# Optimization experiments

Hardware: AMD Instinct MI355X
Metric: run time of the kernel (lower is better)

Reference implementation:

```python
import jax, jax.numpy as jnp
import numpy as np

H = 128  # hidden_dim
F = 64   # node_feat_dim


def setup_inputs() -> dict:
    key = jax.random.key(0)
    ks = jax.random.split(key, 24)
    N, E, NR, NT = 50000, 400000, 20000, 20000
    inp = {
        "mol_x": jax.random.normal(ks[0], (N, F), jnp.float32),
        "pos": jax.random.normal(ks[1], (N, 3), jnp.float32),
        "reaction_x": jax.random.normal(ks[2], (NR, F), jnp.float32),
        "target_x": jax.random.normal(ks[3], (NT, F), jnp.float32),
        "edge_index": jax.random.randint(ks[4], (2, E), 0, N, jnp.int32),
    }
    def lin(k, fan_in, fan_out):
        s = 1.0 / np.sqrt(fan_in)
        kw, kb = jax.random.split(k)
        W = jax.random.uniform(kw, (fan_in, fan_out), jnp.float32, -s, s)
        b = jax.random.uniform(kb, (fan_out,), jnp.float32, -s, s)
        return W, b
    inp["W_node"], inp["b_node"] = lin(ks[5], F, H)
    inp["W_att1"], inp["b_att1"] = lin(ks[6], 2 * H + 3, H)
    inp["W_att2"], inp["b_att2"] = lin(ks[7], H, 1)
    inp["W_upd"], inp["b_upd"] = lin(ks[8], H, H)
    inp["Wy1"], inp["by1"] = lin(ks[9], H, 64)
    inp["Wy2"], inp["by2"] = lin(ks[10], 64, 1)
    inp["Wa1"], inp["ba1"] = lin(ks[11], H, 64)
    inp["Wa2"], inp["ba2"] = lin(ks[12], 64, 1)
    return inp


def reference(mol_x, pos, reaction_x, target_x, edge_index,
              W_node, b_node, W_att1, b_att1, W_att2, b_att2,
              W_upd, b_upd, Wy1, by1, Wy2, by2, Wa1, ba1, Wa2, ba2):
    N = mol_x.shape[0]
    # node encoder
    h = mol_x @ W_node + b_node                      # [N, H]
    src, dst = edge_index[0], edge_index[1]          # PyG: x_j = source, x_i = target
    x_j = h[src]                                      # [E, H]
    x_i = h[dst]                                      # [E, H]
    dist = pos[dst] - pos[src]                        # [E, 3]
    cat = jnp.concatenate([x_i, x_j, dist], axis=1)   # [E, 2H+3]
    s = jax.nn.relu(cat @ W_att1 + b_att1) @ W_att2 + b_att2  # [E, 1]
    att = jax.nn.softmax(s, axis=0)                   # global softmax over edges (dim=0)
    msg = x_j * att                                   # [E, H]
    aggr = jax.ops.segment_sum(msg, dst, num_segments=N)  # scatter-add -> [N, H]
    mol_feats = aggr @ W_upd + b_upd                  # [N, H]
    # heads on reaction / target graphs
    rh = reaction_x @ W_node + b_node
    th = target_x @ W_node + b_node
    pred_yield = (jax.nn.relu(rh @ Wy1 + by1) @ Wy2 + by2).squeeze(-1)
    pred_activity = (jax.nn.relu(th @ Wa1 + ba1) @ Wa2 + ba2).squeeze(-1)
    return pred_yield, pred_activity, mol_feats
```

## Files before the change

### kernel.cpp

```cpp
#include <hip/hip_runtime.h>
#include <hip/hip_bf16.h>

typedef unsigned short ushort_t;
typedef __attribute__((ext_vector_type(8))) short s16x8;
typedef __attribute__((ext_vector_type(4))) float f32x4;

__device__ inline unsigned short f2bf(float x) {
    unsigned u = __float_as_uint(x);
    return (unsigned short)((u + 0x7FFFu + ((u >> 16) & 1u)) >> 16);
}
__device__ inline float bflo(unsigned u) { return __uint_as_float(u << 16); }
__device__ inline float bfhi(unsigned u) { return __uint_as_float(u & 0xffff0000u); }

__device__ inline void pack_one(const float* __restrict__ W, int K, int N,
                                ushort_t* __restrict__ dst, int g) {
    int KT = K / 32;
    int nt = g / (KT * 64);
    int rem = g % (KT * 64);
    int kt = rem / 64, lane = rem % 64;
    int n = nt * 16 + (lane & 15);
    int kbase = kt * 32 + ((lane >> 4) << 3);
    ushort_t tmp[8];
#pragma unroll
    for (int j = 0; j < 8; ++j) tmp[j] = f2bf(W[(size_t)(kbase + j) * N + n]);
    uint4 pk;
    pk.x = tmp[0] | ((unsigned)tmp[1] << 16);
    pk.y = tmp[2] | ((unsigned)tmp[3] << 16);
    pk.z = tmp[4] | ((unsigned)tmp[5] << 16);
    pk.w = tmp[6] | ((unsigned)tmp[7] << 16);
    *(uint4*)&dst[(size_t)g * 8] = pk;
}

__global__ void convert_w(const float* __restrict__ Wn, const float* __restrict__ W1,
                          const float* __restrict__ Wu, const float* __restrict__ Wy1,
                          const float* __restrict__ Wa1,
                          ushort_t* __restrict__ Wnb, ushort_t* __restrict__ W1tb,
                          ushort_t* __restrict__ W1mb, ushort_t* __restrict__ Wub,
                          ushort_t* __restrict__ Wy1b, ushort_t* __restrict__ Wa1b,
                          int* __restrict__ counts, int N) {
    int t = blockIdx.x * 256 + threadIdx.x;
    if (t < 1024)       pack_one(Wn, 64, 128, Wnb, t);
    else if (t < 3072)  pack_one(W1, 128, 128, W1tb, t - 1024);
    else if (t < 5120)  pack_one(W1 + 128 * 128, 128, 128, W1mb, t - 3072);
    else if (t < 7168)  pack_one(Wu, 128, 128, Wub, t - 5120);
    else if (t < 8192)  pack_one(Wy1, 128, 64, Wy1b, t - 7168);
    else if (t < 9216)  pack_one(Wa1, 128, 64, Wa1b, t - 8192);
    if (t < N) counts[t] = 0;
}

__global__ void encode_pq(const float* __restrict__ x, const ushort_t* __restrict__ Wnb,
                          const float* __restrict__ bn, const ushort_t* __restrict__ W1tb,
                          const ushort_t* __restrict__ W1mb, const float* __restrict__ b1,
                          ushort_t* __restrict__ hb, ushort_t* __restrict__ P,
                          ushort_t* __restrict__ Q, int nrows) {
    __shared__ ushort_t ldsH[4 * 16 * 136];
    int t = threadIdx.x;
    int w = t >> 6, lane = t & 63;
    int c = lane & 15, q = lane >> 4;
    int r0 = blockIdx.x * 64 + w * 16;
    int rowA = r0 + c; if (rowA >= nrows) rowA = nrows - 1;
    ushort_t* myH = &ldsH[w * 16 * 136];

    s16x8 xa[2];
#pragma unroll
    for (int kt = 0; kt < 2; ++kt) {
        const float* xp = &x[(size_t)rowA * 64 + kt * 32 + q * 8];
        float4 v0 = *(const float4*)xp;
        float4 v1 = *(const float4*)(xp + 4);
        s16x8 a;
        a[0] = (short)f2bf(v0.x); a[1] = (short)f2bf(v0.y);
        a[2] = (short)f2bf(v0.z); a[3] = (short)f2bf(v0.w);
        a[4] = (short)f2bf(v1.x); a[5] = (short)f2bf(v1.y);
        a[6] = (short)f2bf(v1.z); a[7] = (short)f2bf(v1.w);
        xa[kt] = a;
    }
#pragma unroll
    for (int nt = 0; nt < 8; ++nt) {
        f32x4 acc = {0.f, 0.f, 0.f, 0.f};
#pragma unroll
        for (int kt = 0; kt < 2; ++kt) {
            s16x8 b = *(const s16x8*)&Wnb[((nt * 2 + kt) * 64 + lane) * 8];
            acc = __builtin_amdgcn_mfma_f32_16x16x32_bf16(xa[kt], b, acc, 0, 0, 0);
        }
        float bi = bn[nt * 16 + c];
#pragma unroll
        for (int r = 0; r < 4; ++r) {
            int row = r0 + q * 4 + r;
            ushort_t hv = f2bf(acc[r] + bi);
            myH[(q * 4 + r) * 136 + nt * 16 + c] = hv;
            if (row < nrows) hb[(size_t)row * 128 + nt * 16 + c] = hv;
        }
    }
    __syncthreads();
    s16x8 ha[4];
#pragma unroll
    for (int kt = 0; kt < 4; ++kt)
        ha[kt] = *(const s16x8*)&myH[c * 136 + kt * 32 + q * 8];
#pragma unroll
    for (int nt = 0; nt < 8; ++nt) {
        f32x4 pa = {0.f, 0.f, 0.f, 0.f}, qa = pa;
#pragma unroll
        for (int kt = 0; kt < 4; ++kt) {
            s16x8 bp = *(const s16x8*)&W1tb[((nt * 4 + kt) * 64 + lane) * 8];
            s16x8 bq = *(const s16x8*)&W1mb[((nt * 4 + kt) * 64 + lane) * 8];
            pa = __builtin_amdgcn_mfma_f32_16x16x32_bf16(ha[kt], bp, pa, 0, 0, 0);
            qa = __builtin_amdgcn_mfma_f32_16x16x32_bf16(ha[kt], bq, qa, 0, 0, 0);
        }
        float bi = b1[nt * 16 + c];
#pragma unroll
        for (int r = 0; r < 4; ++r) {
            int row = r0 + q * 4 + r;
            if (row < nrows) {
                P[(size_t)row * 128 + nt * 16 + c] = f2bf(pa[r] + bi);
                Q[(size_t)row * 128 + nt * 16 + c] = f2bf(qa[r]);
            }
        }
    }
}

__global__ void edge_score(const ushort_t* __restrict__ P, const ushort_t* __restrict__ Q,
                           const float* __restrict__ pos, const int* __restrict__ src,
                           const int* __restrict__ dst, const float* __restrict__ W1b,
                           const float* __restrict__ W2, const float* __restrict__ b2,
                           float* __restrict__ s_out, int* __restrict__ counts,
                           float* __restrict__ redm, float* __restrict__ rede, int E) {
    __shared__ float wsh[4 * 128];
    __shared__ float smm[256], sme[256];
    int t = threadIdx.x;
    for (int i = t; i < 384; i += 256) wsh[i] = W1b[i];
    if (t < 128) wsh[384 + t] = W2[t];
    __syncthreads();
    int w = t >> 6, lane = t & 63;
    int g = lane >> 4, c = lane & 15;
    float w0[8], w1[8], w2[8], wv[8];
#pragma unroll
    for (int j = 0; j < 8; ++j) {
        w0[j] = wsh[c * 8 + j];
        w1[j] = wsh[128 + c * 8 + j];
        w2[j] = wsh[256 + c * 8 + j];
        wv[j] = wsh[384 + c * 8 + j];
    }
    float b2v = b2[0];
    int base = blockIdx.x * 64 + w * 16;
    float m = -1e30f, ev = 0.f;

    int sa[4], da[4];
#pragma unroll
    for (int it = 0; it < 4; ++it) {
        int e = base + it * 4 + g;
        int ee = (e < E) ? e : (E - 1);
        sa[it] = src[ee]; da[it] = dst[ee];
    }
    uint4 pr[4], qr[4];
    float dd0[4], dd1[4], dd2[4];
#pragma unroll
    for (int it = 0; it < 4; ++it) {
        pr[it] = *(const uint4*)&P[(size_t)da[it] * 128 + c * 8];
        qr[it] = *(const uint4*)&Q[(size_t)sa[it] * 128 + c * 8];
        dd0[it] = pos[da[it] * 3]     - pos[sa[it] * 3];
        dd1[it] = pos[da[it] * 3 + 1] - pos[sa[it] * 3 + 1];
        dd2[it] = pos[da[it] * 3 + 2] - pos[sa[it] * 3 + 2];
    }
#pragma unroll
    for (int it = 0; it < 4; ++it) {
        int e = base + it * 4 + g;
        bool valid = e < E;
        unsigned pw[4] = {pr[it].x, pr[it].y, pr[it].z, pr[it].w};
        unsigned qw[4] = {qr[it].x, qr[it].y, qr[it].z, qr[it].w};
        float d0 = dd0[it], d1 = dd1[it], d2 = dd2[it];
        float v = 0.f;
#pragma unroll
        for (int jj = 0; jj < 4; ++jj) {
            float pe = bflo(pw[jj]) + bflo(qw[jj])
                     + d0 * w0[2 * jj] + d1 * w1[2 * jj] + d2 * w2[2 * jj];
            float po = bfhi(pw[jj]) + bfhi(qw[jj])
                     + d0 * w0[2 * jj + 1] + d1 * w1[2 * jj + 1] + d2 * w2[2 * jj + 1];
            v += fmaxf(pe, 0.f) * wv[2 * jj] + fmaxf(po, 0.f) * wv[2 * jj + 1];
        }
#pragma unroll
        for (int off = 1; off < 16; off <<= 1) v += __shfl_xor(v, off, 64);
        float sv = v + b2v;
        if (c == 0 && valid) {
            s_out[e] = sv;
            atomicAdd(&counts[da[it]], 1);
            float nm = fmaxf(m, sv);
            ev = ev * __expf(m - nm) + __expf(sv - nm);
            m = nm;
        }
    }
    smm[t] = m; sme[t] = ev; __syncthreads();
    for (int off = 128; off > 0; off >>= 1) {
        if (t < off) {
            float m1 = smm[t], m2 = smm[t + off];
            float e1 = sme[t], e2 = sme[t + off];
            float M = fmaxf(m1, m2);
            smm[t] = M;
            sme[t] = e1 * __expf(m1 - M) + e2 * __expf(m2 - M);
        }
        __syncthreads();
    }
    if (t == 0) { redm[blockIdx.x] = smm[0]; rede[blockIdx.x] = sme[0]; }
}

__global__ void smax2(const float* __restrict__ redm, const float* __restrict__ rede,
                      float* __restrict__ scal, int nb) {
    __shared__ float smm[256], sme[256];
    int t = threadIdx.x;
    float m = -1e30f, ev = 0.f;
    for (int i = t; i < nb; i += 256) {
        float m2 = redm[i], e2 = rede[i];
        float M = fmaxf(m, m2);
        ev = ev * __expf(m - M) + e2 * __expf(m2 - M);
        m = M;
    }
    smm[t] = m; sme[t] = ev; __syncthreads();
    for (int off = 128; off > 0; off >>= 1) {
        if (t < off) {
            float m1 = smm[t], m2 = smm[t + off];
            float e1 = sme[t], e2 = sme[t + off];
            float M = fmaxf(m1, m2);
            smm[t] = M;
            sme[t] = e1 * __expf(m1 - M) + e2 * __expf(m2 - M);
        }
        __syncthreads();
    }
    if (t == 0) { scal[0] = smm[0]; scal[1] = 1.f / sme[0]; }
}

__global__ void scan1(const int* __restrict__ counts, int* __restrict__ offs,
                      int* __restrict__ partials, int N) {
    __shared__ int sm[256];
    int i = blockIdx.x * 256 + threadIdx.x;
    int v = (i < N) ? counts[i] : 0;
    sm[threadIdx.x] = v; __syncthreads();
    for (int off = 1; off < 256; off <<= 1) {
        int add = (threadIdx.x >= off) ? sm[threadIdx.x - off] : 0;
        __syncthreads();
        sm[threadIdx.x] += add;
        __syncthreads();
    }
    if (i < N) offs[i] = sm[threadIdx.x] - v;
    if (threadIdx.x == 255) partials[blockIdx.x] = sm[255];
}

__global__ void scan_add(int* __restrict__ offs, int* __restrict__ cursor,
                         const int* __restrict__ partials, int nb, int N) {
    __shared__ int sm[256];
    int t = threadIdx.x;
    sm[t] = (t < nb && t < blockIdx.x) ? partials[t] : 0;
    __syncthreads();
    for (int off = 128; off > 0; off >>= 1) {
        if (t < off) sm[t] += sm[t + off];
        __syncthreads();
    }
    int basev = sm[0];
    int i = blockIdx.x * 256 + t;
    if (i < N) {
        int v = offs[i] + basev;
        offs[i] = v;
        cursor[i] = v;
    }
}

__global__ void fill_csr(const int* __restrict__ src, const int* __restrict__ dst,
                         const float* __restrict__ s, int* __restrict__ cursor,
                         int2* __restrict__ csr, int E) {
    int e = blockIdx.x * 256 + threadIdx.x;
    if (e >= E) return;
    int p = atomicAdd(&cursor[dst[e]], 1);
    csr[p] = make_int2(src[e], __float_as_int(s[e]));
}

__global__ void gather_upd(const ushort_t* __restrict__ hb, const int2* __restrict__ csr,
                           const int* __restrict__ offs, const int* __restrict__ deg,
                           const float* __restrict__ scal,
                           const ushort_t* __restrict__ Wub, const float* __restrict__ bu,
                           float* __restrict__ C, int N) {
    __shared__ ushort_t ldsA[16 * 136];
    int t = threadIdx.x;
    int w = t >> 6, lane = t & 63;
    int g = lane >> 4, c = lane & 15;
    int r0 = blockIdx.x * 16;
    float m = scal[0], inv = scal[1];
#pragma unroll
    for (int i = 0; i < 4; ++i) {
        int node = r0 + w * 4 + i;
        float a[8] = {0.f, 0.f, 0.f, 0.f, 0.f, 0.f, 0.f, 0.f};
        if (node < N) {
            int start = offs[node], d = deg[node];
            for (int k = g; k < d; k += 4) {
                int2 v = csr[start + k];
                float att = __expf(__int_as_float(v.y) - m) * inv;
                uint4 hq = *(const uint4*)&hb[(size_t)v.x * 128 + c * 8];
                a[0] += bflo(hq.x) * att; a[1] += bfhi(hq.x) * att;
                a[2] += bflo(hq.y) * att; a[3] += bfhi(hq.y) * att;
                a[4] += bflo(hq.z) * att; a[5] += bfhi(hq.z) * att;
                a[6] += bflo(hq.w) * att; a[7] += bfhi(hq.w) * att;
            }
        }
#pragma unroll
        for (int j = 0; j < 8; ++j) {
            a[j] += __shfl_xor(a[j], 16, 64);
            a[j] += __shfl_xor(a[j], 32, 64);
        }
        if (g == 0) {
            uint4 pk;
            pk.x = f2bf(a[0]) | ((unsigned)f2bf(a[1]) << 16);
            pk.y = f2bf(a[2]) | ((unsigned)f2bf(a[3]) << 16);
            pk.z = f2bf(a[4]) | ((unsigned)f2bf(a[5]) << 16);
            pk.w = f2bf(a[6]) | ((unsigned)f2bf(a[7]) << 16);
            *(uint4*)&ldsA[(w * 4 + i) * 136 + c * 8] = pk;
        }
    }
    __syncthreads();
    int q = lane >> 4;
    int ntA = w, ntB = w + 4;
    f32x4 acc0 = {0.f, 0.f, 0.f, 0.f}, acc1 = acc0;
#pragma unroll
    for (int kt = 0; kt < 4; ++kt) {
        s16x8 av = *(const s16x8*)&ldsA[c * 136 + kt * 32 + q * 8];
        s16x8 b0 = *(const s16x8*)&Wub[((ntA * 4 + kt) * 64 + lane) * 8];
        s16x8 b1 = *(const s16x8*)&Wub[((ntB * 4 + kt) * 64 + lane) * 8];
        acc0 = __builtin_amdgcn_mfma_f32_16x16x32_bf16(av, b0, acc0, 0, 0, 0);
        acc1 = __builtin_amdgcn_mfma_f32_16x16x32_bf16(av, b1, acc1, 0, 0, 0);
    }
    float bi0 = bu[ntA * 16 + c], bi1 = bu[ntB * 16 + c];
#pragma unroll
    for (int r = 0; r < 4; ++r) {
        int row = r0 + q * 4 + r;
        if (row < N) {
            C[(size_t)row * 128 + ntA * 16 + c] = acc0[r] + bi0;
            C[(size_t)row * 128 + ntB * 16 + c] = acc1[r] + bi1;
        }
    }
}

__global__ void head_mfma(const float* __restrict__ rx, const float* __restrict__ tx,
                          const ushort_t* __restrict__ Wnb, const float* __restrict__ bn,
                          const ushort_t* __restrict__ Wy1b, const float* __restrict__ by1,
                          const float* __restrict__ Wy2, const float* __restrict__ by2,
                          const ushort_t* __restrict__ Wa1b, const float* __restrict__ ba1,
                          const float* __restrict__ Wa2, const float* __restrict__ ba2,
                          float* __restrict__ out, int nb1, int NR, int NT) {
    __shared__ ushort_t ldsA[16 * 72];
    __shared__ ushort_t ldsB[16 * 136];
    __shared__ float part[64];
    int blk = blockIdx.x;
    const float* x; const ushort_t* W1b; const float* b1; const float* W2; const float* b2;
    float* o; int r0, nrows;
    if (blk < nb1) { x = rx; W1b = Wy1b; b1 = by1; W2 = Wy2; b2 = by2; o = out; r0 = blk * 16; nrows = NR; }
    else { x = tx; W1b = Wa1b; b1 = ba1; W2 = Wa2; b2 = ba2; o = out + NR; r0 = (blk - nb1) * 16; nrows = NT; }

    int t = threadIdx.x;
    {
        int row = t >> 4, c4 = (t & 15) * 4;
        float4 v = *(const float4*)&x[(size_t)(r0 + row) * 64 + c4];
        uint2 pk;
        pk.x = f2bf(v.x) | ((unsigned)f2bf(v.y) << 16);
        pk.y = f2bf(v.z) | ((unsigned)f2bf(v.w) << 16);
        *(uint2*)&ldsA[row * 72 + c4] = pk;
    }
    __syncthreads();
    int w = t >> 6, lane = t & 63;
    int c = lane & 15, q = lane >> 4;
    {
        int ntA = w, ntB = w + 4;
        f32x4 acc0 = {0.f, 0.f, 0.f, 0.f}, acc1 = acc0;
#pragma unroll
        for (int kt = 0; kt < 2; ++kt) {
            s16x8 a = *(const s16x8*)&ldsA[c * 72 + kt * 32 + q * 8];
            s16x8 b0 = *(const s16x8*)&Wnb[((ntA * 2 + kt) * 64 + lane) * 8];
            s16x8 b1v = *(const s16x8*)&Wnb[((ntB * 2 + kt) * 64 + lane) * 8];
            acc0 = __builtin_amdgcn_mfma_f32_16x16x32_bf16(a, b0, acc0, 0, 0, 0);
            acc1 = __builtin_amdgcn_mfma_f32_16x16x32_bf16(a, b1v, acc1, 0, 0, 0);
        }
        float bi0 = bn[ntA * 16 + c], bi1 = bn[ntB * 16 + c];
#pragma unroll
        for (int r = 0; r < 4; ++r) {
            int row = q * 4 + r;
            ldsB[row * 136 + ntA * 16 + c] = f2bf(acc0[r] + bi0);
            ldsB[row * 136 + ntB * 16 + c] = f2bf(acc1[r] + bi1);
        }
    }
    __syncthreads();
    {
        f32x4 acc = {0.f, 0.f, 0.f, 0.f};
#pragma unroll
        for (int kt = 0; kt < 4; ++kt) {
            s16x8 a = *(const s16x8*)&ldsB[c * 136 + kt * 32 + q * 8];
            s16x8 b0 = *(const s16x8*)&W1b[((w * 4 + kt) * 64 + lane) * 8];
            acc = __builtin_amdgcn_mfma_f32_16x16x32_bf16(a, b0, acc, 0, 0, 0);
        }
        float bi = b1[w * 16 + c], w2v = W2[w * 16 + c];
#pragma unroll
        for (int r = 0; r < 4; ++r) {
            float u = fmaxf(acc[r] + bi, 0.f) * w2v;
#pragma unroll
            for (int mm = 1; mm < 16; mm <<= 1) u += __shfl_xor(u, mm, 64);
            if (c == 0) part[w * 16 + q * 4 + r] = u;
        }
    }
    __syncthreads();
    if (t < 16) {
        int row = r0 + t;
        if (row < nrows)
            o[row] = part[t] + part[16 + t] + part[32 + t] + part[48 + t] + b2[0];
    }
}

extern "C" void kernel_launch(void* const* d_in, const int* in_sizes, int n_in,
                              void* d_out, int out_size, void* d_ws, size_t ws_size,
                              hipStream_t stream) {
    const float* mol_x      = (const float*)d_in[0];
    const float* pos        = (const float*)d_in[1];
    const float* reaction_x = (const float*)d_in[2];
    const float* target_x   = (const float*)d_in[3];
    const int*   ei         = (const int*)d_in[4];
    const float* W_node = (const float*)d_in[5];
    const float* b_node = (const float*)d_in[6];
    const float* W_att1 = (const float*)d_in[7];
    const float* b_att1 = (const float*)d_in[8];
    const float* W_att2 = (const float*)d_in[9];
    const float* b_att2 = (const float*)d_in[10];
    const float* W_upd  = (const float*)d_in[11];
    const float* b_upd  = (const float*)d_in[12];
    const float* Wy1 = (const float*)d_in[13];
    const float* by1 = (const float*)d_in[14];
    const float* Wy2 = (const float*)d_in[15];
    const float* by2 = (const float*)d_in[16];
    const float* Wa1 = (const float*)d_in[17];
    const float* ba1 = (const float*)d_in[18];
    const float* Wa2 = (const float*)d_in[19];
    const float* ba2 = (const float*)d_in[20];

    int N  = in_sizes[0] / 64;
    int E  = in_sizes[4] / 2;
    int NR = in_sizes[2] / 64;
    int NT = in_sizes[3] / 64;

    float* out = (float*)d_out;

    int nbE = (E + 63) / 64;

    char* wp = (char*)d_ws;
    ushort_t* hb = (ushort_t*)wp;  wp += (size_t)N * 128 * 2;
    ushort_t* Qb = (ushort_t*)wp;  wp += (size_t)N * 128 * 2;
    float* s     = (float*)wp;     wp += (size_t)E * 4;
    float* redm  = (float*)wp;     wp += (size_t)nbE * 4;
    float* rede  = (float*)wp;     wp += (size_t)nbE * 4;
    float* scal  = (float*)wp;     wp += 4 * 4;
    int* counts  = (int*)wp;       wp += (size_t)N * 4;
    int* offs    = (int*)wp;       wp += (size_t)N * 4;
    int* cursor  = (int*)wp;       wp += (size_t)N * 4;
    int* partials= (int*)wp;       wp += 256 * 4;
    int2* csr    = (int2*)wp;      wp += (size_t)E * 8;
    ushort_t* Wnb  = (ushort_t*)wp; wp += 8192 * 2;
    ushort_t* W1tb = (ushort_t*)wp; wp += 16384 * 2;
    ushort_t* W1mb = (ushort_t*)wp; wp += 16384 * 2;
    ushort_t* Wub  = (ushort_t*)wp; wp += 16384 * 2;
    ushort_t* Wy1b = (ushort_t*)wp; wp += 8192 * 2;
    ushort_t* Wa1b = (ushort_t*)wp; wp += 8192 * 2;
    ushort_t* Pb = (ushort_t*)(out + NR + NT);
    float* molf  = out + NR + NT;

    const int* srcp = ei;
    const int* dstp = ei + E;
    int nbN = (N + 255) / 256;

    convert_w<<<nbN, 256, 0, stream>>>(W_node, W_att1, W_upd, Wy1, Wa1,
                                       Wnb, W1tb, W1mb, Wub, Wy1b, Wa1b, counts, N);
    encode_pq<<<(N + 63) / 64, 256, 0, stream>>>(mol_x, Wnb, b_node, W1tb, W1mb, b_att1,
                                                 hb, Pb, Qb, N);
    edge_score<<<nbE, 256, 0, stream>>>(Pb, Qb, pos, srcp, dstp,
                                        W_att1 + 256 * 128, W_att2, b_att2,
                                        s, counts, redm, rede, E);
    smax2<<<1, 256, 0, stream>>>(redm, rede, scal, nbE);
    scan1<<<nbN, 256, 0, stream>>>(counts, offs, partials, N);
    scan_add<<<nbN, 256, 0, stream>>>(offs, cursor, partials, nbN, N);
    fill_csr<<<(E + 255) / 256, 256, 0, stream>>>(srcp, dstp, s, cursor, csr, E);
    gather_upd<<<(N + 15) / 16, 256, 0, stream>>>(hb, csr, offs, counts, scal,
                                                  Wub, b_upd, molf, N);
    head_mfma<<<(NR + NT) / 16, 256, 0, stream>>>(reaction_x, target_x, Wnb, b_node,
                                                  Wy1b, by1, Wy2, by2, Wa1b, ba1, Wa2, ba2,
                                                  out, NR / 16, NR, NT);
}
```

Measured before the change: 249.3 us.

## Fuse edge scoring into CSR gather with per-node online softmax

Removes the separate edge_score pass: attention scores are now computed inside the destination-sorted gather, which keeps a per-node running max and sum and rescales the aggregated features. A global softmax rescale factor per node is applied after the W_upd MFMA, and the degree counting moves into encode_pq. Q and h are interleaved in one row so each source gather touches a single 512-byte region, and the CSR stores only source indices. The trade-off is a serialized per-node loop doing more exp work, a larger per-source read, and the risk of underflow in the per-node scaling for nodes whose max is far below the global max.

```diff
diff --git a/kernel.cpp b/kernel.cpp
--- a/kernel.cpp
+++ b/kernel.cpp
@@ -51,10 +51,13 @@
 __global__ void encode_pq(const float* __restrict__ x, const ushort_t* __restrict__ Wnb,
                           const float* __restrict__ bn, const ushort_t* __restrict__ W1tb,
                           const ushort_t* __restrict__ W1mb, const float* __restrict__ b1,
-                          ushort_t* __restrict__ hb, ushort_t* __restrict__ P,
-                          ushort_t* __restrict__ Q, int nrows) {
+                          ushort_t* __restrict__ QH, ushort_t* __restrict__ P,
+                          const int* __restrict__ dst, int* __restrict__ counts,
+                          int nrows, int E) {
     __shared__ ushort_t ldsH[4 * 16 * 136];
     int t = threadIdx.x;
+    for (int e = blockIdx.x * 256 + t; e < E; e += gridDim.x * 256)
+        atomicAdd(&counts[dst[e]], 1);
     int w = t >> 6, lane = t & 63;
     int c = lane & 15, q = lane >> 4;
     int r0 = blockIdx.x * 64 + w * 16;
@@ -88,7 +91,7 @@
             int row = r0 + q * 4 + r;
             ushort_t hv = f2bf(acc[r] + bi);
             myH[(q * 4 + r) * 136 + nt * 16 + c] = hv;
-            if (row < nrows) hb[(size_t)row * 128 + nt * 16 + c] = hv;
+            if (row < nrows) QH[(size_t)row * 256 + 128 + nt * 16 + c] = hv;
         }
     }
     __syncthreads();
@@ -112,119 +115,10 @@
             int row = r0 + q * 4 + r;
             if (row < nrows) {
                 P[(size_t)row * 128 + nt * 16 + c] = f2bf(pa[r] + bi);
-                Q[(size_t)row * 128 + nt * 16 + c] = f2bf(qa[r]);
+                QH[(size_t)row * 256 + nt * 16 + c] = f2bf(qa[r]);
             }
         }
     }
-}
-
-__global__ void edge_score(const ushort_t* __restrict__ P, const ushort_t* __restrict__ Q,
-                           const float* __restrict__ pos, const int* __restrict__ src,
-                           const int* __restrict__ dst, const float* __restrict__ W1b,
-                           const float* __restrict__ W2, const float* __restrict__ b2,
-                           float* __restrict__ s_out, int* __restrict__ counts,
-                           float* __restrict__ redm, float* __restrict__ rede, int E) {
-    __shared__ float wsh[4 * 128];
-    __shared__ float smm[256], sme[256];
-    int t = threadIdx.x;
-    for (int i = t; i < 384; i += 256) wsh[i] = W1b[i];
-    if (t < 128) wsh[384 + t] = W2[t];
-    __syncthreads();
-    int w = t >> 6, lane = t & 63;
-    int g = lane >> 4, c = lane & 15;
-    float w0[8], w1[8], w2[8], wv[8];
-#pragma unroll
-    for (int j = 0; j < 8; ++j) {
-        w0[j] = wsh[c * 8 + j];
-        w1[j] = wsh[128 + c * 8 + j];
-        w2[j] = wsh[256 + c * 8 + j];
-        wv[j] = wsh[384 + c * 8 + j];
-    }
-    float b2v = b2[0];
-    int base = blockIdx.x * 64 + w * 16;
-    float m = -1e30f, ev = 0.f;
-
-    int sa[4], da[4];
-#pragma unroll
-    for (int it = 0; it < 4; ++it) {
-        int e = base + it * 4 + g;
-        int ee = (e < E) ? e : (E - 1);
-        sa[it] = src[ee]; da[it] = dst[ee];
-    }
-    uint4 pr[4], qr[4];
-    float dd0[4], dd1[4], dd2[4];
-#pragma unroll
-    for (int it = 0; it < 4; ++it) {
-        pr[it] = *(const uint4*)&P[(size_t)da[it] * 128 + c * 8];
-        qr[it] = *(const uint4*)&Q[(size_t)sa[it] * 128 + c * 8];
-        dd0[it] = pos[da[it] * 3]     - pos[sa[it] * 3];
-        dd1[it] = pos[da[it] * 3 + 1] - pos[sa[it] * 3 + 1];
-        dd2[it] = pos[da[it] * 3 + 2] - pos[sa[it] * 3 + 2];
-    }
-#pragma unroll
-    for (int it = 0; it < 4; ++it) {
-        int e = base + it * 4 + g;
-        bool valid = e < E;
-        unsigned pw[4] = {pr[it].x, pr[it].y, pr[it].z, pr[it].w};
-        unsigned qw[4] = {qr[it].x, qr[it].y, qr[it].z, qr[it].w};
-        float d0 = dd0[it], d1 = dd1[it], d2 = dd2[it];
-        float v = 0.f;
-#pragma unroll
-        for (int jj = 0; jj < 4; ++jj) {
-            float pe = bflo(pw[jj]) + bflo(qw[jj])
-                     + d0 * w0[2 * jj] + d1 * w1[2 * jj] + d2 * w2[2 * jj];
-            float po = bfhi(pw[jj]) + bfhi(qw[jj])
-                     + d0 * w0[2 * jj + 1] + d1 * w1[2 * jj + 1] + d2 * w2[2 * jj + 1];
-            v += fmaxf(pe, 0.f) * wv[2 * jj] + fmaxf(po, 0.f) * wv[2 * jj + 1];
-        }
-#pragma unroll
-        for (int off = 1; off < 16; off <<= 1) v += __shfl_xor(v, off, 64);
-        float sv = v + b2v;
-        if (c == 0 && valid) {
-            s_out[e] = sv;
-            atomicAdd(&counts[da[it]], 1);
-            float nm = fmaxf(m, sv);
-            ev = ev * __expf(m - nm) + __expf(sv - nm);
-            m = nm;
-        }
-    }
-    smm[t] = m; sme[t] = ev; __syncthreads();
-    for (int off = 128; off > 0; off >>= 1) {
-        if (t < off) {
-            float m1 = smm[t], m2 = smm[t + off];
-            float e1 = sme[t], e2 = sme[t + off];
-            float M = fmaxf(m1, m2);
-            smm[t] = M;
-            sme[t] = e1 * __expf(m1 - M) + e2 * __expf(m2 - M);
-        }
-        __syncthreads();
-    }
-    if (t == 0) { redm[blockIdx.x] = smm[0]; rede[blockIdx.x] = sme[0]; }
-}
-
-__global__ void smax2(const float* __restrict__ redm, const float* __restrict__ rede,
-                      float* __restrict__ scal, int nb) {
-    __shared__ float smm[256], sme[256];
-    int t = threadIdx.x;
-    float m = -1e30f, ev = 0.f;
-    for (int i = t; i < nb; i += 256) {
-        float m2 = redm[i], e2 = rede[i];
-        float M = fmaxf(m, m2);
-        ev = ev * __expf(m - M) + e2 * __expf(m2 - M);
-        m = M;
-    }
-    smm[t] = m; sme[t] = ev; __syncthreads();
-    for (int off = 128; off > 0; off >>= 1) {
-        if (t < off) {
-            float m1 = smm[t], m2 = smm[t + off];
-            float e1 = sme[t], e2 = sme[t + off];
-            float M = fmaxf(m1, m2);
-            smm[t] = M;
-            sme[t] = e1 * __expf(m1 - M) + e2 * __expf(m2 - M);
-        }
-        __syncthreads();
-    }
-    if (t == 0) { scal[0] = smm[0]; scal[1] = 1.f / sme[0]; }
 }
 
 __global__ void scan1(const int* __restrict__ counts, int* __restrict__ offs,
@@ -263,57 +157,166 @@
 }
 
 __global__ void fill_csr(const int* __restrict__ src, const int* __restrict__ dst,
-                         const float* __restrict__ s, int* __restrict__ cursor,
-                         int2* __restrict__ csr, int E) {
+                         int* __restrict__ cursor, int* __restrict__ csrc, int E) {
     int e = blockIdx.x * 256 + threadIdx.x;
     if (e >= E) return;
     int p = atomicAdd(&cursor[dst[e]], 1);
-    csr[p] = make_int2(src[e], __float_as_int(s[e]));
-}
-
-__global__ void gather_upd(const ushort_t* __restrict__ hb, const int2* __restrict__ csr,
-                           const int* __restrict__ offs, const int* __restrict__ deg,
-                           const float* __restrict__ scal,
-                           const ushort_t* __restrict__ Wub, const float* __restrict__ bu,
-                           float* __restrict__ C, int N) {
-    __shared__ ushort_t ldsA[16 * 136];
-    int t = threadIdx.x;
+    csrc[p] = src[e];
+}
+
+__global__ void fused_gather(const ushort_t* __restrict__ P, const ushort_t* __restrict__ QH,
+                             const float* __restrict__ pos, const int* __restrict__ csrc,
+                             const int* __restrict__ offs, const int* __restrict__ deg,
+                             const float* __restrict__ W1b, const float* __restrict__ W2,
+                             const float* __restrict__ b2,
+                             ushort_t* __restrict__ A_out, float* __restrict__ m_out,
+                             float* __restrict__ redm, float* __restrict__ rede, int N) {
+    __shared__ float wsh[512];
+    __shared__ float smm[256], sme[256];
+    int t = threadIdx.x;
+    for (int i = t; i < 384; i += 256) wsh[i] = W1b[i];
+    if (t < 128) wsh[384 + t] = W2[t];
+    __syncthreads();
     int w = t >> 6, lane = t & 63;
     int g = lane >> 4, c = lane & 15;
-    int r0 = blockIdx.x * 16;
-    float m = scal[0], inv = scal[1];
+    float w0[8], w1[8], w2[8], wv[8];
+#pragma unroll
+    for (int j = 0; j < 8; ++j) {
+        w0[j] = wsh[c * 8 + j];
+        w1[j] = wsh[128 + c * 8 + j];
+        w2[j] = wsh[256 + c * 8 + j];
+        wv[j] = wsh[384 + c * 8 + j];
+    }
+    float b2v = b2[0];
+    float mB = -1e30f, zB = 0.f;
 #pragma unroll
     for (int i = 0; i < 4; ++i) {
-        int node = r0 + w * 4 + i;
+        int node = blockIdx.x * 16 + w * 4 + i;
+        float m = -1e30f, z = 0.f;
         float a[8] = {0.f, 0.f, 0.f, 0.f, 0.f, 0.f, 0.f, 0.f};
         if (node < N) {
+            uint4 pr = *(const uint4*)&P[(size_t)node * 128 + c * 8];
+            float pv[8];
+            pv[0] = bflo(pr.x); pv[1] = bfhi(pr.x); pv[2] = bflo(pr.y); pv[3] = bfhi(pr.y);
+            pv[4] = bflo(pr.z); pv[5] = bfhi(pr.z); pv[6] = bflo(pr.w); pv[7] = bfhi(pr.w);
+            float pd0 = pos[node * 3], pd1 = pos[node * 3 + 1], pd2 = pos[node * 3 + 2];
             int start = offs[node], d = deg[node];
             for (int k = g; k < d; k += 4) {
-                int2 v = csr[start + k];
-                float att = __expf(__int_as_float(v.y) - m) * inv;
-                uint4 hq = *(const uint4*)&hb[(size_t)v.x * 128 + c * 8];
-                a[0] += bflo(hq.x) * att; a[1] += bfhi(hq.x) * att;
-                a[2] += bflo(hq.y) * att; a[3] += bfhi(hq.y) * att;
-                a[4] += bflo(hq.z) * att; a[5] += bfhi(hq.z) * att;
-                a[6] += bflo(hq.w) * att; a[7] += bfhi(hq.w) * att;
+                int sa = csrc[start + k];
+                const ushort_t* qhp = &QH[(size_t)sa * 256 + c * 8];
+                uint4 qr = *(const uint4*)qhp;
+                uint4 hr = *(const uint4*)(qhp + 128);
+                float d0 = pd0 - pos[sa * 3];
+                float d1 = pd1 - pos[sa * 3 + 1];
+                float d2 = pd2 - pos[sa * 3 + 2];
+                unsigned qw[4] = {qr.x, qr.y, qr.z, qr.w};
+                float v = 0.f;
+#pragma unroll
+                for (int jj = 0; jj < 4; ++jj) {
+                    float pe = pv[2 * jj] + bflo(qw[jj])
+                             + d0 * w0[2 * jj] + d1 * w1[2 * jj] + d2 * w2[2 * jj];
+                    float po = pv[2 * jj + 1] + bfhi(qw[jj])
+                             + d0 * w0[2 * jj + 1] + d1 * w1[2 * jj + 1] + d2 * w2[2 * jj + 1];
+                    v += fmaxf(pe, 0.f) * wv[2 * jj] + fmaxf(po, 0.f) * wv[2 * jj + 1];
+                }
+#pragma unroll
+                for (int off = 1; off < 16; off <<= 1) v += __shfl_xor(v, off, 64);
+                float s = v + b2v;
+                float nm = fmaxf(m, s);
+                float f  = __expf(m - nm);
+                float es = __expf(s - nm);
+                z = z * f + es;
+                m = nm;
+                float hv[8];
+                hv[0] = bflo(hr.x); hv[1] = bfhi(hr.x); hv[2] = bflo(hr.y); hv[3] = bfhi(hr.y);
+                hv[4] = bflo(hr.z); hv[5] = bfhi(hr.z); hv[6] = bflo(hr.w); hv[7] = bfhi(hr.w);
+#pragma unroll
+                for (int j = 0; j < 8; ++j) a[j] = a[j] * f + hv[j] * es;
             }
         }
 #pragma unroll
-        for (int j = 0; j < 8; ++j) {
-            a[j] += __shfl_xor(a[j], 16, 64);
-            a[j] += __shfl_xor(a[j], 32, 64);
-        }
-        if (g == 0) {
+        for (int off = 16; off <= 32; off <<= 1) {
+            float m2 = __shfl_xor(m, off, 64);
+            float z2 = __shfl_xor(z, off, 64);
+            float M = fmaxf(m, m2);
+            float e1 = __expf(m - M), e2 = __expf(m2 - M);
+#pragma unroll
+            for (int j = 0; j < 8; ++j) {
+                float a2 = __shfl_xor(a[j], off, 64);
+                a[j] = a[j] * e1 + a2 * e2;
+            }
+            z = z * e1 + z2 * e2;
+            m = M;
+        }
+        if (g == 0 && node < N) {
             uint4 pk;
             pk.x = f2bf(a[0]) | ((unsigned)f2bf(a[1]) << 16);
             pk.y = f2bf(a[2]) | ((unsigned)f2bf(a[3]) << 16);
             pk.z = f2bf(a[4]) | ((unsigned)f2bf(a[5]) << 16);
             pk.w = f2bf(a[6]) | ((unsigned)f2bf(a[7]) << 16);
-            *(uint4*)&ldsA[(w * 4 + i) * 136 + c * 8] = pk;
-        }
-    }
-    __syncthreads();
-    int q = lane >> 4;
+            *(uint4*)&A_out[(size_t)node * 128 + c * 8] = pk;
+            if (c == 0) {
+                m_out[node] = m;
+                float M = fmaxf(mB, m);
+                float e1 = __expf(mB - M), e2 = __expf(m - M);
+                zB = zB * e1 + z * e2;
+                mB = M;
+            }
+        }
+    }
+    smm[t] = mB; sme[t] = zB; __syncthreads();
+    for (int off = 128; off > 0; off >>= 1) {
+        if (t < off) {
+            float m1 = smm[t], m2 = smm[t + off];
+            float e1 = sme[t], e2 = sme[t + off];
+            float M = fmaxf(m1, m2);
+            smm[t] = M;
+            sme[t] = e1 * __expf(m1 - M) + e2 * __expf(m2 - M);
+        }
+        __syncthreads();
+    }
+    if (t == 0) { redm[blockIdx.x] = smm[0]; rede[blockIdx.x] = sme[0]; }
+}
+
+__global__ void combine(const float* __restrict__ redm, const float* __restrict__ rede,
+                        float* __restrict__ scal, int nb) {
+    __shared__ float smm[256], sme[256];
+    int t = threadIdx.x;
+    float m = -1e30f, ev = 0.f;
+    for (int i = t; i < nb; i += 256) {
+        float m2 = redm[i], e2 = rede[i];
+        float M = fmaxf(m, m2);
+        ev = ev * __expf(m - M) + e2 * __expf(m2 - M);
+        m = M;
+    }
+    smm[t] = m; sme[t] = ev; __syncthreads();
+    for (int off = 128; off > 0; off >>= 1) {
+        if (t < off) {
+            float m1 = smm[t], m2 = smm[t + off];
+            float e1 = sme[t], e2 = sme[t + off];
+            float M = fmaxf(m1, m2);
+            smm[t] = M;
+            sme[t] = e1 * __expf(m1 - M) + e2 * __expf(m2 - M);
+        }
+        __syncthreads();
+    }
+    if (t == 0) { scal[0] = smm[0]; scal[1] = 1.f / sme[0]; }
+}
+
+__global__ void upd_mfma(const ushort_t* __restrict__ A, const float* __restrict__ m_n,
+                         const float* __restrict__ scal,
+                         const ushort_t* __restrict__ Wub, const float* __restrict__ bu,
+                         float* __restrict__ C, int N) {
+    __shared__ ushort_t ldsA[16 * 136];
+    int t = threadIdx.x;
+    int r0 = blockIdx.x * 16;
+    {
+        int row = t >> 4, c8 = (t & 15) * 8;
+        *(uint4*)&ldsA[row * 136 + c8] = *(const uint4*)&A[(size_t)(r0 + row) * 128 + c8];
+    }
+    __syncthreads();
+    int w = t >> 6, lane = t & 63;
+    int c = lane & 15, q = lane >> 4;
     int ntA = w, ntB = w + 4;
     f32x4 acc0 = {0.f, 0.f, 0.f, 0.f}, acc1 = acc0;
 #pragma unroll
@@ -324,13 +327,15 @@
         acc0 = __builtin_amdgcn_mfma_f32_16x16x32_bf16(av, b0, acc0, 0, 0, 0);
         acc1 = __builtin_amdgcn_mfma_f32_16x16x32_bf16(av, b1, acc1, 0, 0, 0);
     }
+    float M = scal[0], invZ = scal[1];
     float bi0 = bu[ntA * 16 + c], bi1 = bu[ntB * 16 + c];
 #pragma unroll
     for (int r = 0; r < 4; ++r) {
         int row = r0 + q * 4 + r;
         if (row < N) {
-            C[(size_t)row * 128 + ntA * 16 + c] = acc0[r] + bi0;
-            C[(size_t)row * 128 + ntB * 16 + c] = acc1[r] + bi1;
+            float sc = __expf(m_n[row] - M) * invZ;
+            C[(size_t)row * 128 + ntA * 16 + c] = acc0[r] * sc + bi0;
+            C[(size_t)row * 128 + ntB * 16 + c] = acc1[r] * sc + bi1;
         }
     }
 }
@@ -440,20 +445,20 @@
 
     float* out = (float*)d_out;
 
-    int nbE = (E + 63) / 64;
+    int nbG = (N + 15) / 16;
 
     char* wp = (char*)d_ws;
-    ushort_t* hb = (ushort_t*)wp;  wp += (size_t)N * 128 * 2;
-    ushort_t* Qb = (ushort_t*)wp;  wp += (size_t)N * 128 * 2;
-    float* s     = (float*)wp;     wp += (size_t)E * 4;
-    float* redm  = (float*)wp;     wp += (size_t)nbE * 4;
-    float* rede  = (float*)wp;     wp += (size_t)nbE * 4;
+    ushort_t* QH = (ushort_t*)wp;  wp += (size_t)N * 256 * 2;
+    ushort_t* Ab = (ushort_t*)wp;  wp += (size_t)N * 128 * 2;
+    float* m_n   = (float*)wp;     wp += (size_t)N * 4;
+    float* redm  = (float*)wp;     wp += (size_t)nbG * 4;
+    float* rede  = (float*)wp;     wp += (size_t)nbG * 4;
     float* scal  = (float*)wp;     wp += 4 * 4;
     int* counts  = (int*)wp;       wp += (size_t)N * 4;
     int* offs    = (int*)wp;       wp += (size_t)N * 4;
     int* cursor  = (int*)wp;       wp += (size_t)N * 4;
     int* partials= (int*)wp;       wp += 256 * 4;
-    int2* csr    = (int2*)wp;      wp += (size_t)E * 8;
+    int* csrc    = (int*)wp;       wp += (size_t)E * 4;
     ushort_t* Wnb  = (ushort_t*)wp; wp += 8192 * 2;
     ushort_t* W1tb = (ushort_t*)wp; wp += 16384 * 2;
     ushort_t* W1mb = (ushort_t*)wp; wp += 16384 * 2;
@@ -470,16 +475,15 @@
     convert_w<<<nbN, 256, 0, stream>>>(W_node, W_att1, W_upd, Wy1, Wa1,
                                        Wnb, W1tb, W1mb, Wub, Wy1b, Wa1b, counts, N);
     encode_pq<<<(N + 63) / 64, 256, 0, stream>>>(mol_x, Wnb, b_node, W1tb, W1mb, b_att1,
-                                                 hb, Pb, Qb, N);
-    edge_score<<<nbE, 256, 0, stream>>>(Pb, Qb, pos, srcp, dstp,
-                                        W_att1 + 256 * 128, W_att2, b_att2,
-                                        s, counts, redm, rede, E);
-    smax2<<<1, 256, 0, stream>>>(redm, rede, scal, nbE);
+                                                 QH, Pb, dstp, counts, N, E);
     scan1<<<nbN, 256, 0, stream>>>(counts, offs, partials, N);
     scan_add<<<nbN, 256, 0, stream>>>(offs, cursor, partials, nbN, N);
-    fill_csr<<<(E + 255) / 256, 256, 0, stream>>>(srcp, dstp, s, cursor, csr, E);
-    gather_upd<<<(N + 15) / 16, 256, 0, stream>>>(hb, csr, offs, counts, scal,
-                                                  Wub, b_upd, molf, N);
+    fill_csr<<<(E + 255) / 256, 256, 0, stream>>>(srcp, dstp, cursor, csrc, E);
+    fused_gather<<<nbG, 256, 0, stream>>>(Pb, QH, pos, csrc, offs, counts,
+                                          W_att1 + 256 * 128, W_att2, b_att2,
+                                          Ab, m_n, redm, rede, N);
+    combine<<<1, 256, 0, stream>>>(redm, rede, scal, nbG);
+    upd_mfma<<<(N + 15) / 16, 256, 0, stream>>>(Ab, m_n, scal, Wub, b_upd, molf, N);
     head_mfma<<<(NR + NT) / 16, 256, 0, stream>>>(reaction_x, target_x, Wnb, b_node,
                                                   Wy1b, by1, Wy2, by2, Wa1b, ba1, Wa2, ba2,
                                                   out, NR / 16, NR, NT);
```

After: 268.0 us. 1.08x slower.

## Move degree counting into encoder and fuse CSR fill into edge scoring

Applied to the files above, without the earlier changes.

The per-destination degree histogram is now built with atomics inside the encoder kernel, and the scan runs before edge scoring. The edge-score kernel then writes (src, score) pairs straight into CSR slots, which removes the separate fill_csr kernel and the intermediate score buffer. The cost is extra atomic traffic in the encoder and scattered CSR writes inside the scoring kernel. The gather loop in edge_score was also restructured from batched loads into a per-iteration loop, which may reduce memory-level parallelism.

```diff
diff --git a/kernel.cpp b/kernel.cpp
--- a/kernel.cpp
+++ b/kernel.cpp
@@ -52,9 +52,12 @@
                           const float* __restrict__ bn, const ushort_t* __restrict__ W1tb,
                           const ushort_t* __restrict__ W1mb, const float* __restrict__ b1,
                           ushort_t* __restrict__ hb, ushort_t* __restrict__ P,
-                          ushort_t* __restrict__ Q, int nrows) {
+                          ushort_t* __restrict__ Q, const int* __restrict__ dst,
+                          int* __restrict__ counts, int nrows, int E) {
     __shared__ ushort_t ldsH[4 * 16 * 136];
     int t = threadIdx.x;
+    for (int e = blockIdx.x * 256 + t; e < E; e += gridDim.x * 256)
+        atomicAdd(&counts[dst[e]], 1);
     int w = t >> 6, lane = t & 63;
     int c = lane & 15, q = lane >> 4;
     int r0 = blockIdx.x * 64 + w * 16;
@@ -116,115 +119,6 @@
             }
         }
     }
-}
-
-__global__ void edge_score(const ushort_t* __restrict__ P, const ushort_t* __restrict__ Q,
-                           const float* __restrict__ pos, const int* __restrict__ src,
-                           const int* __restrict__ dst, const float* __restrict__ W1b,
-                           const float* __restrict__ W2, const float* __restrict__ b2,
-                           float* __restrict__ s_out, int* __restrict__ counts,
-                           float* __restrict__ redm, float* __restrict__ rede, int E) {
-    __shared__ float wsh[4 * 128];
-    __shared__ float smm[256], sme[256];
-    int t = threadIdx.x;
-    for (int i = t; i < 384; i += 256) wsh[i] = W1b[i];
-    if (t < 128) wsh[384 + t] = W2[t];
-    __syncthreads();
-    int w = t >> 6, lane = t & 63;
-    int g = lane >> 4, c = lane & 15;
-    float w0[8], w1[8], w2[8], wv[8];
-#pragma unroll
-    for (int j = 0; j < 8; ++j) {
-        w0[j] = wsh[c * 8 + j];
-        w1[j] = wsh[128 + c * 8 + j];
-        w2[j] = wsh[256 + c * 8 + j];
-        wv[j] = wsh[384 + c * 8 + j];
-    }
-    float b2v = b2[0];
-    int base = blockIdx.x * 64 + w * 16;
-    float m = -1e30f, ev = 0.f;
-
-    int sa[4], da[4];
-#pragma unroll
-    for (int it = 0; it < 4; ++it) {
-        int e = base + it * 4 + g;
-        int ee = (e < E) ? e : (E - 1);
-        sa[it] = src[ee]; da[it] = dst[ee];
-    }
-    uint4 pr[4], qr[4];
-    float dd0[4], dd1[4], dd2[4];
-#pragma unroll
-    for (int it = 0; it < 4; ++it) {
-        pr[it] = *(const uint4*)&P[(size_t)da[it] * 128 + c * 8];
-        qr[it] = *(const uint4*)&Q[(size_t)sa[it] * 128 + c * 8];
-        dd0[it] = pos[da[it] * 3]     - pos[sa[it] * 3];
-        dd1[it] = pos[da[it] * 3 + 1] - pos[sa[it] * 3 + 1];
-        dd2[it] = pos[da[it] * 3 + 2] - pos[sa[it] * 3 + 2];
-    }
-#pragma unroll
-    for (int it = 0; it < 4; ++it) {
-        int e = base + it * 4 + g;
-        bool valid = e < E;
-        unsigned pw[4] = {pr[it].x, pr[it].y, pr[it].z, pr[it].w};
-        unsigned qw[4] = {qr[it].x, qr[it].y, qr[it].z, qr[it].w};
-        float d0 = dd0[it], d1 = dd1[it], d2 = dd2[it];
-        float v = 0.f;
-#pragma unroll
-        for (int jj = 0; jj < 4; ++jj) {
-            float pe = bflo(pw[jj]) + bflo(qw[jj])
-                     + d0 * w0[2 * jj] + d1 * w1[2 * jj] + d2 * w2[2 * jj];
-            float po = bfhi(pw[jj]) + bfhi(qw[jj])
-                     + d0 * w0[2 * jj + 1] + d1 * w1[2 * jj + 1] + d2 * w2[2 * jj + 1];
-            v += fmaxf(pe, 0.f) * wv[2 * jj] + fmaxf(po, 0.f) * wv[2 * jj + 1];
-        }
-#pragma unroll
-        for (int off = 1; off < 16; off <<= 1) v += __shfl_xor(v, off, 64);
-        float sv = v + b2v;
-        if (c == 0 && valid) {
-            s_out[e] = sv;
-            atomicAdd(&counts[da[it]], 1);
-            float nm = fmaxf(m, sv);
-            ev = ev * __expf(m - nm) + __expf(sv - nm);
-            m = nm;
-        }
-    }
-    smm[t] = m; sme[t] = ev; __syncthreads();
-    for (int off = 128; off > 0; off >>= 1) {
-        if (t < off) {
-            float m1 = smm[t], m2 = smm[t + off];
-            float e1 = sme[t], e2 = sme[t + off];
-            float M = fmaxf(m1, m2);
-            smm[t] = M;
-            sme[t] = e1 * __expf(m1 - M) + e2 * __expf(m2 - M);
-        }
-        __syncthreads();
-    }
-    if (t == 0) { redm[blockIdx.x] = smm[0]; rede[blockIdx.x] = sme[0]; }
-}
-
-__global__ void smax2(const float* __restrict__ redm, const float* __restrict__ rede,
-                      float* __restrict__ scal, int nb) {
-    __shared__ float smm[256], sme[256];
-    int t = threadIdx.x;
-    float m = -1e30f, ev = 0.f;
-    for (int i = t; i < nb; i += 256) {
-        float m2 = redm[i], e2 = rede[i];
-        float M = fmaxf(m, m2);
-        ev = ev * __expf(m - M) + e2 * __expf(m2 - M);
-        m = M;
-    }
-    smm[t] = m; sme[t] = ev; __syncthreads();
-    for (int off = 128; off > 0; off >>= 1) {
-        if (t < off) {
-            float m1 = smm[t], m2 = smm[t + off];
-            float e1 = sme[t], e2 = sme[t + off];
-            float M = fmaxf(m1, m2);
-            smm[t] = M;
-            sme[t] = e1 * __expf(m1 - M) + e2 * __expf(m2 - M);
-        }
-        __syncthreads();
-    }
-    if (t == 0) { scal[0] = smm[0]; scal[1] = 1.f / sme[0]; }
 }
 
 __global__ void scan1(const int* __restrict__ counts, int* __restrict__ offs,
@@ -262,13 +156,101 @@
     }
 }
 
-__global__ void fill_csr(const int* __restrict__ src, const int* __restrict__ dst,
-                         const float* __restrict__ s, int* __restrict__ cursor,
-                         int2* __restrict__ csr, int E) {
-    int e = blockIdx.x * 256 + threadIdx.x;
-    if (e >= E) return;
-    int p = atomicAdd(&cursor[dst[e]], 1);
-    csr[p] = make_int2(src[e], __float_as_int(s[e]));
+__global__ void edge_score(const ushort_t* __restrict__ P, const ushort_t* __restrict__ Q,
+                           const float* __restrict__ pos, const int* __restrict__ src,
+                           const int* __restrict__ dst, const float* __restrict__ W1b,
+                           const float* __restrict__ W2, const float* __restrict__ b2,
+                           int* __restrict__ cursor, int2* __restrict__ csr,
+                           float* __restrict__ redm, float* __restrict__ rede, int E) {
+    __shared__ float wsh[512];
+    __shared__ float smm[256], sme[256];
+    int t = threadIdx.x;
+    for (int i = t; i < 384; i += 256) wsh[i] = W1b[i];
+    if (t < 128) wsh[384 + t] = W2[t];
+    __syncthreads();
+    int w = t >> 6, lane = t & 63;
+    int g = lane >> 4, c = lane & 15;
+    float w0[8], w1[8], w2[8], wv[8];
+#pragma unroll
+    for (int j = 0; j < 8; ++j) {
+        w0[j] = wsh[c * 8 + j];
+        w1[j] = wsh[128 + c * 8 + j];
+        w2[j] = wsh[256 + c * 8 + j];
+        wv[j] = wsh[384 + c * 8 + j];
+    }
+    float b2v = b2[0];
+    int base = blockIdx.x * 64 + w * 16;
+    float m = -1e30f, ev = 0.f;
+#pragma unroll
+    for (int it = 0; it < 4; ++it) {
+        int e = base + it * 4 + g;
+        bool valid = e < E;
+        int ee = valid ? e : (E - 1);
+        int sa = src[ee], da = dst[ee];
+        uint4 pr = *(const uint4*)&P[(size_t)da * 128 + c * 8];
+        uint4 qr = *(const uint4*)&Q[(size_t)sa * 128 + c * 8];
+        float d0 = pos[da * 3]     - pos[sa * 3];
+        float d1 = pos[da * 3 + 1] - pos[sa * 3 + 1];
+        float d2 = pos[da * 3 + 2] - pos[sa * 3 + 2];
+        unsigned pw[4] = {pr.x, pr.y, pr.z, pr.w};
+        unsigned qw[4] = {qr.x, qr.y, qr.z, qr.w};
+        float v = 0.f;
+#pragma unroll
+        for (int jj = 0; jj < 4; ++jj) {
+            float pe = bflo(pw[jj]) + bflo(qw[jj])
+                     + d0 * w0[2 * jj] + d1 * w1[2 * jj] + d2 * w2[2 * jj];
+            float po = bfhi(pw[jj]) + bfhi(qw[jj])
+                     + d0 * w0[2 * jj + 1] + d1 * w1[2 * jj + 1] + d2 * w2[2 * jj + 1];
+            v += fmaxf(pe, 0.f) * wv[2 * jj] + fmaxf(po, 0.f) * wv[2 * jj + 1];
+        }
+#pragma unroll
+        for (int off = 1; off < 16; off <<= 1) v += __shfl_xor(v, off, 64);
+        if (c == 0 && valid) {
+            float sv = v + b2v;
+            int p = atomicAdd(&cursor[da], 1);
+            csr[p] = make_int2(sa, __float_as_int(sv));
+            float nm = fmaxf(m, sv);
+            ev = ev * __expf(m - nm) + __expf(sv - nm);
+            m = nm;
+        }
+    }
+    smm[t] = m; sme[t] = ev; __syncthreads();
+    for (int off = 128; off > 0; off >>= 1) {
+        if (t < off) {
+            float m1 = smm[t], m2 = smm[t + off];
+            float e1 = sme[t], e2 = sme[t + off];
+            float M = fmaxf(m1, m2);
+            smm[t] = M;
+            sme[t] = e1 * __expf(m1 - M) + e2 * __expf(m2 - M);
+        }
+        __syncthreads();
+    }
+    if (t == 0) { redm[blockIdx.x] = smm[0]; rede[blockIdx.x] = sme[0]; }
+}
+
+__global__ void smax2(const float* __restrict__ redm, const float* __restrict__ rede,
+                      float* __restrict__ scal, int nb) {
+    __shared__ float smm[256], sme[256];
+    int t = threadIdx.x;
+    float m = -1e30f, ev = 0.f;
+    for (int i = t; i < nb; i += 256) {
+        float m2 = redm[i], e2 = rede[i];
+        float M = fmaxf(m, m2);
+        ev = ev * __expf(m - M) + e2 * __expf(m2 - M);
+        m = M;
+    }
+    smm[t] = m; sme[t] = ev; __syncthreads();
+    for (int off = 128; off > 0; off >>= 1) {
+        if (t < off) {
+            float m1 = smm[t], m2 = smm[t + off];
+            float e1 = sme[t], e2 = sme[t + off];
+            float M = fmaxf(m1, m2);
+            smm[t] = M;
+            sme[t] = e1 * __expf(m1 - M) + e2 * __expf(m2 - M);
+        }
+        __syncthreads();
+    }
+    if (t == 0) { scal[0] = smm[0]; scal[1] = 1.f / sme[0]; }
 }
 
 __global__ void gather_upd(const ushort_t* __restrict__ hb, const int2* __restrict__ csr,
@@ -445,7 +427,6 @@
     char* wp = (char*)d_ws;
     ushort_t* hb = (ushort_t*)wp;  wp += (size_t)N * 128 * 2;
     ushort_t* Qb = (ushort_t*)wp;  wp += (size_t)N * 128 * 2;
-    float* s     = (float*)wp;     wp += (size_t)E * 4;
     float* redm  = (float*)wp;     wp += (size_t)nbE * 4;
     float* rede  = (float*)wp;     wp += (size_t)nbE * 4;
     float* scal  = (float*)wp;     wp += 4 * 4;
@@ -470,14 +451,13 @@
     convert_w<<<nbN, 256, 0, stream>>>(W_node, W_att1, W_upd, Wy1, Wa1,
                                        Wnb, W1tb, W1mb, Wub, Wy1b, Wa1b, counts, N);
     encode_pq<<<(N + 63) / 64, 256, 0, stream>>>(mol_x, Wnb, b_node, W1tb, W1mb, b_att1,
-                                                 hb, Pb, Qb, N);
+                                                 hb, Pb, Qb, dstp, counts, N, E);
+    scan1<<<nbN, 256, 0, stream>>>(counts, offs, partials, N);
+    scan_add<<<nbN, 256, 0, stream>>>(offs, cursor, partials, nbN, N);
     edge_score<<<nbE, 256, 0, stream>>>(Pb, Qb, pos, srcp, dstp,
                                         W_att1 + 256 * 128, W_att2, b_att2,
-                                        s, counts, redm, rede, E);
+                                        cursor, csr, redm, rede, E);
     smax2<<<1, 256, 0, stream>>>(redm, rede, scal, nbE);
-    scan1<<<nbN, 256, 0, stream>>>(counts, offs, partials, N);
-    scan_add<<<nbN, 256, 0, stream>>>(offs, cursor, partials, nbN, N);
-    fill_csr<<<(E + 255) / 256, 256, 0, stream>>>(srcp, dstp, s, cursor, csr, E);
     gather_upd<<<(N + 15) / 16, 256, 0, stream>>>(hb, csr, offs, counts, scal,
                                                   Wub, b_upd, molf, N);
     head_mfma<<<(NR + NT) / 16, 256, 0, stream>>>(reaction_x, target_x, Wnb, b_node,
```

Measured after the change: 246.9 us. Within noise of the previous version (-1.0%).
